# Kernel optimization log

Hardware: AMD Instinct MI355X
Metric: run time of the kernel (lower is better)

## Reference

```python
import jax, jax.numpy as jnp
import numpy as np
from jax import lax

B, N, D = 16, 2048, 256
H = 64  # hidden_dim
EPS = 1e-5


def zero_softmax(x, eps=EPS):
    # zeros stay exactly zero: exp(0)-1 == 0
    e = jnp.exp(x) - 1.0
    return e / (jnp.sum(e, axis=-1, keepdims=True) + eps)


def setup_inputs() -> dict:
    key = jax.random.key(0)
    ks = jax.random.split(key, 9)
    s_in = 1.0 / np.sqrt(D)
    x = jax.random.normal(ks[0], (B, N, D), dtype=jnp.float32)
    Wq = jax.random.uniform(ks[1], (D, H), jnp.float32, -s_in, s_in)
    bq = jax.random.uniform(ks[2], (H,), jnp.float32, -s_in, s_in)
    Wk = jax.random.uniform(ks[3], (D, H), jnp.float32, -s_in, s_in)
    bk = jax.random.uniform(ks[4], (H,), jnp.float32, -s_in, s_in)
    Wv = jax.random.uniform(ks[5], (D, H), jnp.float32, -s_in, s_in)
    bv = jax.random.uniform(ks[6], (H,), jnp.float32, -s_in, s_in)
    s_c = 1.0 / 3.0  # conv fan_in = 1*3*3 = 9
    conv_w = jax.random.uniform(ks[7], (1, 1, 3, 3), jnp.float32, -s_c, s_c)
    conv_b = jax.random.uniform(ks[8], (1,), jnp.float32, -s_c, s_c)
    return {"x": x, "Wq": Wq, "bq": bq, "Wk": Wk, "bk": bk,
            "Wv": Wv, "bv": bv, "conv_w": conv_w, "conv_b": conv_b}


def reference(x, Wq, bq, Wk, bk, Wv, bv, conv_w, conv_b):
    scale = H ** (-0.5)
    q = jnp.einsum('bnd,dh->bnh', x, Wq) + bq
    k = jnp.einsum('bnd,dh->bnh', x, Wk) + bk
    v = jnp.einsum('bnd,dh->bnh', x, Wv) + bv
    A_dense = jnp.einsum('bnh,bmh->bnm', q, k) * scale  # [B, N, N]
    A_in = A_dense[:, None, :, :]  # [B, 1, N, N]
    A_conv = lax.conv_general_dilated(
        A_in, conv_w, window_strides=(1, 1), padding='SAME',
        dimension_numbers=('NCHW', 'OIHW', 'NCHW')) + conv_b[None, :, None, None]
    A_conv = jax.nn.sigmoid(A_conv)[:, 0, :, :]
    A_sparse = jax.nn.relu(A_dense - A_conv)
    A_norm = zero_softmax(A_sparse)
    return jnp.einsum('bnm,bmh->bnh', A_norm, v)
```

## Files before the change

kernel.cpp:

```cpp
#include <hip/hip_runtime.h>
#include <hip/hip_bf16.h>

typedef __bf16 bf16_t;
typedef __bf16 bf16x8 __attribute__((ext_vector_type(8)));
typedef float  floatx4 __attribute__((ext_vector_type(4)));

#define BQ 16
#define NTOK 2048

__global__ __launch_bounds__(256) void k_prep(const float* __restrict__ Wq,
                                              const float* __restrict__ Wk,
                                              const float* __restrict__ Wv,
                                              bf16_t* __restrict__ wt,
                                              float* __restrict__ outz,
                                              float* __restrict__ rsz) {
    int o = blockIdx.x * 256 + threadIdx.x;
    if (o < 49152) {
        int w = o >> 14;
        int r = o & 16383;
        int h = r >> 8;
        int d = r & 255;
        const float* W = (w == 0) ? Wq : ((w == 1) ? Wk : Wv);
        wt[o] = (bf16_t)W[d * 64 + h];
    }
    float4 z = make_float4(0.f, 0.f, 0.f, 0.f);
    for (int u = o; u < 532480; u += 262144) {
        if (u < 524288) ((float4*)outz)[u] = z;
        else            ((float4*)rsz)[u - 524288] = z;
    }
}

#define XS 264
#define VS 40
__global__ __launch_bounds__(256) void k_qkv(const float* __restrict__ x,
                                             const bf16_t* __restrict__ wt,
                                             const float* __restrict__ bq,
                                             const float* __restrict__ bk,
                                             const float* __restrict__ bv,
                                             bf16_t* __restrict__ qb,
                                             bf16_t* __restrict__ kb,
                                             bf16_t* __restrict__ vt) {
    __shared__ bf16_t x_ls[32 * XS];
    __shared__ bf16_t vt_ls[64 * VS];

    int b  = blockIdx.x >> 6;
    int t0 = (blockIdx.x & 63) << 5;
    int t  = threadIdx.x;
    int lane = t & 63;
    int w    = t >> 6;
    int m_   = lane & 15;
    int q4   = lane >> 4;

    for (int tau = t; tau < 2048; tau += 256) {
        int row = tau >> 6, ch = tau & 63;
        float4 v = ((const float4*)x)[(size_t)(b * NTOK + t0 + row) * 64 + ch];
        bf16_t tmp[4] = {(bf16_t)v.x, (bf16_t)v.y, (bf16_t)v.z, (bf16_t)v.w};
        *(uint2*)(&x_ls[row * XS + ch * 4]) = *(uint2*)tmp;
    }
    __syncthreads();

    for (int wi = 0; wi < 3; ++wi) {
        const bf16_t* wtw = wt + wi * 16384;
        floatx4 acc[2];
        #pragma unroll
        for (int mt = 0; mt < 2; ++mt) acc[mt] = floatx4{0.f, 0.f, 0.f, 0.f};

        #pragma unroll
        for (int ks = 0; ks < 8; ++ks) {
            bf16x8 bfrag = *(const bf16x8*)(wtw + (16 * w + m_) * 256 + ks * 32 + q4 * 8);
            #pragma unroll
            for (int mt = 0; mt < 2; ++mt) {
                bf16x8 afrag = *(const bf16x8*)(&x_ls[(16 * mt + m_) * XS + ks * 32 + q4 * 8]);
                acc[mt] = __builtin_amdgcn_mfma_f32_16x16x32_bf16(afrag, bfrag, acc[mt], 0, 0, 0);
            }
        }
        const float* bias_p = (wi == 0) ? bq : ((wi == 1) ? bk : bv);
        float bias = bias_p[16 * w + m_];
        float scale = (wi == 0) ? 0.125f : 1.0f;

        if (wi < 2) {
            bf16_t* dst = (wi == 0) ? qb : kb;
            #pragma unroll
            for (int mt = 0; mt < 2; ++mt)
                #pragma unroll
                for (int r = 0; r < 4; ++r) {
                    int tok = t0 + 16 * mt + 4 * q4 + r;
                    dst[(size_t)(b * NTOK + tok) * 64 + 16 * w + m_] = (bf16_t)((acc[mt][r] + bias) * scale);
                }
        } else {
            #pragma unroll
            for (int mt = 0; mt < 2; ++mt)
                #pragma unroll
                for (int r = 0; r < 4; ++r)
                    vt_ls[(16 * w + m_) * VS + 16 * mt + 4 * q4 + r] = (bf16_t)(acc[mt][r] + bias);
            __syncthreads();
            {
                int h = t >> 2, ch = t & 3;
                uint4 val = *(const uint4*)(&vt_ls[h * VS + ch * 8]);
                *(uint4*)(vt + (size_t)(b * 64 + h) * NTOK + t0 + ch * 8) = val;
            }
        }
    }
}

#define PS 72
#define NITC 34
#define CHUNK 12
#define GX 45
__global__ __launch_bounds__(256) void k_attn(const bf16_t* __restrict__ qb,
                                              const bf16_t* __restrict__ kb,
                                              const bf16_t* __restrict__ vt,
                                              const float* __restrict__ conv_w,
                                              const float* __restrict__ conv_b,
                                              float* __restrict__ outp,
                                              float* __restrict__ rsg) {
    __shared__ __align__(16) char smem[12288];
    bf16_t* pls    = (bf16_t*)smem;
    float*  seamG0 = (float*)(smem + 6912);
    float*  seamG2 = (float*)(smem + 7680);
    float*  scr    = (float*)smem;

    int b  = blockIdx.z;
    int bx = blockIdx.x;
    int it0   = blockIdx.y * CHUNK;
    int itEnd = (it0 + CHUNK < NITC) ? (it0 + CHUNK) : NITC;
    int t = threadIdx.x, lane = t & 63, w = t >> 6;
    int m_ = lane & 15, q4 = lane >> 4;

    float cw[9];
    #pragma unroll
    for (int i = 0; i < 9; ++i) cw[i] = conv_w[i];
    float cb = conv_b[0];

    bf16x8 qf[3][2];
    {
        int tokq = 46 * bx - 1 + m_;
        #pragma unroll
        for (int si = 0; si < 3; ++si) {
            int tok = tokq + 16 * si;
            bool ok = (tok >= 0) && (tok < NTOK);
            #pragma unroll
            for (int ks = 0; ks < 2; ++ks) {
                bf16x8 v = {};
                if (ok) v = *(const bf16x8*)(qb + ((size_t)(b * NTOK + tok)) * 64 + ks * 32 + q4 * 8);
                qf[si][ks] = v;
            }
        }
    }

    bool rimcol = ((w == 0) && (m_ == 0)) || ((w == 3) && (m_ == 15));

    floatx4 accO[3];
    #pragma unroll
    for (int si = 0; si < 3; ++si) accO[si] = floatx4{0.f, 0.f, 0.f, 0.f};
    float rs[3][4] = {};

    const bf16_t* kbb = kb + (size_t)b * NTOK * 64;
    const bf16_t* vtb = vt + (size_t)b * 64 * NTOK;
    size_t vrow = (size_t)(16 * w + m_) * NTOK;

    bf16x8 kf[2], vf[2];
    auto load_kv = [&](int it, bf16x8* kd, bf16x8* vd) {
        int fs = 62 * it - 2;
        int tok = fs + 16 * w + m_;
        bool ok = (tok >= 0) && (tok < NTOK);
        #pragma unroll
        for (int ks = 0; ks < 2; ++ks) {
            bf16x8 v = {};
            if (ok) v = *(const bf16x8*)(kbb + (size_t)tok * 64 + ks * 32 + q4 * 8);
            kd[ks] = v;
        }
        #pragma unroll
        for (int ks = 0; ks < 2; ++ks) {
            int col = fs + 32 * ks + 8 * q4;
            if (col < 0 || col > NTOK - 8) {
                bf16x8 v = {};
                #pragma unroll
                for (int j = 0; j < 8; ++j) {
                    int tk = col + j;
                    if (tk >= 0 && tk < NTOK) v[j] = vtb[vrow + tk];
                }
                vd[ks] = v;
            } else {
                vd[ks] = *(const bf16x8*)(vtb + vrow + col);
            }
        }
    };
    load_kv(it0, kf, vf);

    for (int it = it0; it < itEnd; ++it) {
        floatx4 Cq[3];
        #pragma unroll
        for (int si = 0; si < 3; ++si) {
            floatx4 c = floatx4{0.f, 0.f, 0.f, 0.f};
            #pragma unroll
            for (int ks = 0; ks < 2; ++ks)
                c = __builtin_amdgcn_mfma_f32_16x16x32_bf16(qf[si][ks], kf[ks], c, 0, 0, 0);
            Cq[si] = c;
        }

        float cp[3][4];
        #pragma unroll
        for (int si = 0; si < 3; ++si) {
            float a_up = __shfl(Cq[si][3], lane - 16);
            float b_up = (si > 0) ? __shfl(Cq[si - 1][3], lane + 48) : 0.f;
            float c_dn = __shfl(Cq[si][0], lane + 16);
            float d_dn = (si < 2) ? __shfl(Cq[si + 1][0], lane - 48) : 0.f;
            float up[4], dn[4];
            up[0] = (q4 > 0) ? a_up : b_up;
            up[1] = Cq[si][0]; up[2] = Cq[si][1]; up[3] = Cq[si][2];
            dn[0] = Cq[si][1]; dn[1] = Cq[si][2]; dn[2] = Cq[si][3];
            dn[3] = (q4 < 3) ? c_dn : d_dn;

            float G0[4], G1[4], G2[4];
            #pragma unroll
            for (int r = 0; r < 4; ++r) {
                float cu = Cq[si][r];
                G0[r] = cw[0] * up[r] + cw[3] * cu + cw[6] * dn[r];
                G1[r] = cw[1] * up[r] + cw[4] * cu + cw[7] * dn[r];
                G2[r] = cw[2] * up[r] + cw[5] * cu + cw[8] * dn[r];
            }
            #pragma unroll
            for (int r = 0; r < 4; ++r) {
                float e0 = __shfl(G0[r], lane - 1);
                float e2 = __shfl(G2[r], lane + 1);
                cp[si][r] = G1[r] + ((m_ >= 1) ? e0 : 0.f) + ((m_ <= 14) ? e2 : 0.f);
            }
            if (m_ == 15) {
                float4 tv = make_float4(G0[0], G0[1], G0[2], G0[3]);
                *(float4*)&seamG0[w * 48 + 16 * si + 4 * q4] = tv;
            }
            if (m_ == 0) {
                float4 tv = make_float4(G2[0], G2[1], G2[2], G2[3]);
                *(float4*)&seamG2[w * 48 + 16 * si + 4 * q4] = tv;
            }
        }
        __syncthreads();

        bf16x8 kn[2] = {}, vn[2] = {};
        bool pf = (it + 1 < itEnd);
        if (pf) load_kv(it + 1, kn, vn);

        #pragma unroll
        for (int si = 0; si < 3; ++si) {
            if (m_ == 0 && w > 0) {
                float4 s0 = *(const float4*)&seamG0[(w - 1) * 48 + 16 * si + 4 * q4];
                cp[si][0] += s0.x; cp[si][1] += s0.y; cp[si][2] += s0.z; cp[si][3] += s0.w;
            }
            if (m_ == 15 && w < 3) {
                float4 s2 = *(const float4*)&seamG2[(w + 1) * 48 + 16 * si + 4 * q4];
                cp[si][0] += s2.x; cp[si][1] += s2.y; cp[si][2] += s2.z; cp[si][3] += s2.w;
            }
            #pragma unroll
            for (int r = 0; r < 4; ++r) {
                float conv = cp[si][r] + cb;
                float sig = __builtin_amdgcn_rcpf(1.f + __expf(-conv));
                float s = fmaxf(Cq[si][r] - sig, 0.f);
                float ev = __expf(s) - 1.f;
                if (rimcol) ev = 0.f;
                rs[si][r] += ev;
                pls[(16 * si + 4 * q4 + r) * PS + 16 * w + m_] = (bf16_t)ev;
            }
        }
        __syncthreads();

        #pragma unroll
        for (int ks = 0; ks < 2; ++ks)
            #pragma unroll
            for (int si = 0; si < 3; ++si) {
                bf16x8 af = *(const bf16x8*)(pls + (16 * si + m_) * PS + ks * 32 + q4 * 8);
                accO[si] = __builtin_amdgcn_mfma_f32_16x16x32_bf16(af, vf[ks], accO[si], 0, 0, 0);
            }
        if (pf) {
            #pragma unroll
            for (int ks = 0; ks < 2; ++ks) { kf[ks] = kn[ks]; vf[ks] = vn[ks]; }
        }
    }

    __syncthreads();
    #pragma unroll
    for (int si = 0; si < 3; ++si)
        #pragma unroll
        for (int r = 0; r < 4; ++r)
            scr[(16 * si + 4 * q4 + r) * 64 + 16 * w + m_] = rs[si][r];
    __syncthreads();
    if (t < 46) {
        int grow = 46 * bx + t;
        if (grow < NTOK) {
            const float4* p4 = (const float4*)(scr + (t + 1) * 64);
            float s = 0.f;
            #pragma unroll
            for (int j = 0; j < 16; ++j) { float4 v = p4[j]; s += v.x + v.y + v.z + v.w; }
            atomicAdd(&rsg[b * NTOK + grow], s);
        }
    }
    #pragma unroll
    for (int si = 0; si < 3; ++si)
        #pragma unroll
        for (int r = 0; r < 4; ++r) {
            int f = 16 * si + 4 * q4 + r;
            int grow = 46 * bx - 1 + f;
            if (f >= 1 && f < 47 && grow < NTOK)
                atomicAdd(outp + ((size_t)(b * NTOK + grow)) * 64 + 16 * w + m_, accO[si][r]);
        }
}

__global__ __launch_bounds__(256) void k_norm(float* __restrict__ out,
                                              const float* __restrict__ rsg) {
    int gid = blockIdx.x * 256 + threadIdx.x;
    float4 o = ((float4*)out)[gid];
    float d = rsg[gid >> 4] + 1e-5f;
    float inv = 1.f / d;
    o.x *= inv; o.y *= inv; o.z *= inv; o.w *= inv;
    ((float4*)out)[gid] = o;
}

extern "C" void kernel_launch(void* const* d_in, const int* in_sizes, int n_in,
                              void* d_out, int out_size, void* d_ws, size_t ws_size,
                              hipStream_t stream) {
    const float* x  = (const float*)d_in[0];
    const float* Wq = (const float*)d_in[1];
    const float* bq = (const float*)d_in[2];
    const float* Wk = (const float*)d_in[3];
    const float* bk = (const float*)d_in[4];
    const float* Wv = (const float*)d_in[5];
    const float* bv = (const float*)d_in[6];
    const float* cw = (const float*)d_in[7];
    const float* cb = (const float*)d_in[8];
    float* out = (float*)d_out;

    char* ws = (char*)d_ws;
    bf16_t* wt = (bf16_t*)ws;
    bf16_t* qb = (bf16_t*)(ws + 98304);
    bf16_t* kb = (bf16_t*)(ws + 98304 + 4194304);
    bf16_t* vt = (bf16_t*)(ws + 98304 + 8388608);
    float*  rsg = (float*)(ws + 98304 + 12582912);

    k_prep<<<dim3(1024), dim3(256), 0, stream>>>(Wq, Wk, Wv, wt, out, rsg);
    k_qkv<<<dim3(1024), dim3(256), 0, stream>>>(x, wt, bq, bk, bv, qb, kb, vt);
    k_attn<<<dim3(GX, 3, BQ), dim3(256), 0, stream>>>(qb, kb, vt, cw, cb, out, rsg);
    k_norm<<<dim3(2048), dim3(256), 0, stream>>>(out, rsg);
}
```

Measured before the change: 240.0 us.

## Give each wave independent overlapping key windows to drop per-iteration block barriers

Each wave now handles its own 14-column key window with one-column halos on both sides, so the 3x3 conv seams are covered inside the wave. This removes the shared seam buffers and the two __syncthreads per iteration. Each wave keeps a private P tile in LDS and computes all 64 hidden columns of P·V, which takes four accumulator sets per row slice. Partial outputs are reduced across waves in LDS at the end, then written with one atomic per element. In exchange the halo columns are recomputed, V is loaded every iteration without prefetch, register pressure goes up, and there are more iterations (37 vs 34).

After: 378.3 us. +57.6%, slower.

```diff
diff --git a/kernel.cpp b/kernel.cpp
--- a/kernel.cpp
+++ b/kernel.cpp
@@ -103,9 +103,8 @@
     }
 }
 
-#define PS 72
-#define NITC 34
-#define CHUNK 12
+#define PST 40
+#define NIT 37
 #define GX 45
 __global__ __launch_bounds__(256) void k_attn(const bf16_t* __restrict__ qb,
                                               const bf16_t* __restrict__ kb,
@@ -114,24 +113,25 @@
                                               const float* __restrict__ conv_b,
                                               float* __restrict__ outp,
                                               float* __restrict__ rsg) {
-    __shared__ __align__(16) char smem[12288];
-    bf16_t* pls    = (bf16_t*)smem;
-    float*  seamG0 = (float*)(smem + 6912);
-    float*  seamG2 = (float*)(smem + 7680);
-    float*  scr    = (float*)smem;
+    __shared__ __align__(16) char smem[15360];
 
     int b  = blockIdx.z;
     int bx = blockIdx.x;
-    int it0   = blockIdx.y * CHUNK;
-    int itEnd = (it0 + CHUNK < NITC) ? (it0 + CHUNK) : NITC;
+    int it0   = blockIdx.y * 13;
+    int itEnd = (it0 + 13 < NIT) ? (it0 + 13) : NIT;
     int t = threadIdx.x, lane = t & 63, w = t >> 6;
     int m_ = lane & 15, q4 = lane >> 4;
+
+    bf16_t* pls = (bf16_t*)smem + w * (48 * PST);
+    float*  scr = (float*)smem;
 
     float cw[9];
     #pragma unroll
     for (int i = 0; i < 9; ++i) cw[i] = conv_w[i];
     float cb = conv_b[0];
 
+    for (int u = lane; u < 48 * PST / 2; u += 64) ((uint*)pls)[u] = 0u;
+
     bf16x8 qf[3][2];
     {
         int tokq = 46 * bx - 1 + m_;
@@ -148,21 +148,21 @@
         }
     }
 
-    bool rimcol = ((w == 0) && (m_ == 0)) || ((w == 3) && (m_ == 15));
-
-    floatx4 accO[3];
+    floatx4 accO[3][4];
     #pragma unroll
-    for (int si = 0; si < 3; ++si) accO[si] = floatx4{0.f, 0.f, 0.f, 0.f};
+    for (int si = 0; si < 3; ++si)
+        #pragma unroll
+        for (int th = 0; th < 4; ++th) accO[si][th] = floatx4{0.f, 0.f, 0.f, 0.f};
     float rs[3][4] = {};
 
     const bf16_t* kbb = kb + (size_t)b * NTOK * 64;
     const bf16_t* vtb = vt + (size_t)b * 64 * NTOK;
-    size_t vrow = (size_t)(16 * w + m_) * NTOK;
-
-    bf16x8 kf[2], vf[2];
-    auto load_kv = [&](int it, bf16x8* kd, bf16x8* vd) {
-        int fs = 62 * it - 2;
-        int tok = fs + 16 * w + m_;
+
+    bool pmask = (m_ == 0) || (m_ == 15);
+
+    auto load_k = [&](int it, bf16x8* kd) {
+        int aw0 = 56 * it - 1 + 14 * w;
+        int tok = aw0 + m_;
         bool ok = (tok >= 0) && (tok < NTOK);
         #pragma unroll
         for (int ks = 0; ks < 2; ++ks) {
@@ -170,25 +170,34 @@
             if (ok) v = *(const bf16x8*)(kbb + (size_t)tok * 64 + ks * 32 + q4 * 8);
             kd[ks] = v;
         }
-        #pragma unroll
-        for (int ks = 0; ks < 2; ++ks) {
-            int col = fs + 32 * ks + 8 * q4;
+    };
+    auto load_v = [&](int it, bf16x8* vd) {
+        int aw0 = 56 * it - 1 + 14 * w;
+        int col = aw0 + 8 * q4;
+        #pragma unroll
+        for (int th = 0; th < 4; ++th) {
+            size_t hrow = (size_t)(16 * th + m_) * NTOK;
             if (col < 0 || col > NTOK - 8) {
                 bf16x8 v = {};
                 #pragma unroll
                 for (int j = 0; j < 8; ++j) {
                     int tk = col + j;
-                    if (tk >= 0 && tk < NTOK) v[j] = vtb[vrow + tk];
+                    if (tk >= 0 && tk < NTOK) v[j] = vtb[hrow + tk];
                 }
-                vd[ks] = v;
+                vd[th] = v;
             } else {
-                vd[ks] = *(const bf16x8*)(vtb + vrow + col);
+                vd[th] = *(const bf16x8*)(vtb + hrow + col);
             }
         }
     };
-    load_kv(it0, kf, vf);
+
+    bf16x8 kf[2];
+    load_k(it0, kf);
 
     for (int it = it0; it < itEnd; ++it) {
+        bf16x8 vf[4];
+        load_v(it, vf);
+
         floatx4 Cq[3];
         #pragma unroll
         for (int si = 0; si < 3; ++si) {
@@ -199,7 +208,10 @@
             Cq[si] = c;
         }
 
-        float cp[3][4];
+        bf16x8 kn[2] = {};
+        bool pf = (it + 1 < itEnd);
+        if (pf) load_k(it + 1, kn);
+
         #pragma unroll
         for (int si = 0; si < 3; ++si) {
             float a_up = __shfl(Cq[si][3], lane - 16);
@@ -224,59 +236,50 @@
             for (int r = 0; r < 4; ++r) {
                 float e0 = __shfl(G0[r], lane - 1);
                 float e2 = __shfl(G2[r], lane + 1);
-                cp[si][r] = G1[r] + ((m_ >= 1) ? e0 : 0.f) + ((m_ <= 14) ? e2 : 0.f);
-            }
-            if (m_ == 15) {
-                float4 tv = make_float4(G0[0], G0[1], G0[2], G0[3]);
-                *(float4*)&seamG0[w * 48 + 16 * si + 4 * q4] = tv;
-            }
-            if (m_ == 0) {
-                float4 tv = make_float4(G2[0], G2[1], G2[2], G2[3]);
-                *(float4*)&seamG2[w * 48 + 16 * si + 4 * q4] = tv;
-            }
-        }
-        __syncthreads();
-
-        bf16x8 kn[2] = {}, vn[2] = {};
-        bool pf = (it + 1 < itEnd);
-        if (pf) load_kv(it + 1, kn, vn);
-
-        #pragma unroll
-        for (int si = 0; si < 3; ++si) {
-            if (m_ == 0 && w > 0) {
-                float4 s0 = *(const float4*)&seamG0[(w - 1) * 48 + 16 * si + 4 * q4];
-                cp[si][0] += s0.x; cp[si][1] += s0.y; cp[si][2] += s0.z; cp[si][3] += s0.w;
-            }
-            if (m_ == 15 && w < 3) {
-                float4 s2 = *(const float4*)&seamG2[(w + 1) * 48 + 16 * si + 4 * q4];
-                cp[si][0] += s2.x; cp[si][1] += s2.y; cp[si][2] += s2.z; cp[si][3] += s2.w;
-            }
-            #pragma unroll
-            for (int r = 0; r < 4; ++r) {
-                float conv = cp[si][r] + cb;
+                float conv = G1[r] + e0 + e2 + cb;
                 float sig = __builtin_amdgcn_rcpf(1.f + __expf(-conv));
                 float s = fmaxf(Cq[si][r] - sig, 0.f);
                 float ev = __expf(s) - 1.f;
-                if (rimcol) ev = 0.f;
+                if (pmask) ev = 0.f;
                 rs[si][r] += ev;
-                pls[(16 * si + 4 * q4 + r) * PS + 16 * w + m_] = (bf16_t)ev;
-            }
+                pls[(16 * si + 4 * q4 + r) * PST + m_] = (bf16_t)ev;
+            }
+        }
+
+        #pragma unroll
+        for (int si = 0; si < 3; ++si) {
+            bf16x8 af = *(const bf16x8*)(pls + (16 * si + m_) * PST + 8 * q4);
+            #pragma unroll
+            for (int th = 0; th < 4; ++th)
+                accO[si][th] = __builtin_amdgcn_mfma_f32_16x16x32_bf16(af, vf[th], accO[si][th], 0, 0, 0);
+        }
+
+        if (pf) { kf[0] = kn[0]; kf[1] = kn[1]; }
+    }
+
+    __syncthreads();
+    #pragma unroll
+    for (int ww = 0; ww < 4; ++ww) {
+        if (w == ww) {
+            #pragma unroll
+            for (int si = 0; si < 3; ++si)
+                #pragma unroll
+                for (int th = 0; th < 4; ++th)
+                    #pragma unroll
+                    for (int r = 0; r < 4; ++r) {
+                        int idx = (16 * si + 4 * q4 + r) * 64 + 16 * th + m_;
+                        if (ww == 0) scr[idx] = accO[si][th][r];
+                        else         scr[idx] += accO[si][th][r];
+                    }
         }
         __syncthreads();
-
-        #pragma unroll
-        for (int ks = 0; ks < 2; ++ks)
-            #pragma unroll
-            for (int si = 0; si < 3; ++si) {
-                bf16x8 af = *(const bf16x8*)(pls + (16 * si + m_) * PS + ks * 32 + q4 * 8);
-                accO[si] = __builtin_amdgcn_mfma_f32_16x16x32_bf16(af, vf[ks], accO[si], 0, 0, 0);
-            }
-        if (pf) {
-            #pragma unroll
-            for (int ks = 0; ks < 2; ++ks) { kf[ks] = kn[ks]; vf[ks] = vn[ks]; }
-        }
-    }
-
+    }
+    for (int e = t; e < 2944; e += 256) {
+        int f = (e >> 6) + 1, h = e & 63;
+        int grow = 46 * bx + f - 1;
+        if (grow < NTOK)
+            atomicAdd(outp + ((size_t)(b * NTOK + grow)) * 64 + h, scr[f * 64 + h]);
+    }
     __syncthreads();
     #pragma unroll
     for (int si = 0; si < 3; ++si)
@@ -294,15 +297,6 @@
             atomicAdd(&rsg[b * NTOK + grow], s);
         }
     }
-    #pragma unroll
-    for (int si = 0; si < 3; ++si)
-        #pragma unroll
-        for (int r = 0; r < 4; ++r) {
-            int f = 16 * si + 4 * q4 + r;
-            int grow = 46 * bx - 1 + f;
-            if (f >= 1 && f < 47 && grow < NTOK)
-                atomicAdd(outp + ((size_t)(b * NTOK + grow)) * 64 + 16 * w + m_, accO[si][r]);
-        }
 }
 
 __global__ __launch_bounds__(256) void k_norm(float* __restrict__ out,
```
